# Optimization experiments

Hardware: AMD Instinct MI355X
Metric: run time of the kernel (lower is better)

The kernel has to match this reference:

```python
import jax, jax.numpy as jnp
import numpy as np

K_NEIGHBORS = 32
BN_EPS = 1e-5


def setup_inputs() -> dict:
    key = jax.random.key(0)
    ks = jax.random.split(key, 5)
    B, N, C, OUT = 16, 2048, 3, 32
    x = jax.random.normal(ks[0], (B, N, C), dtype=jnp.float32)
    W1 = jax.random.normal(ks[1], (2 * C, 2 * C), dtype=jnp.float32) * 0.3
    b1 = jax.random.normal(ks[2], (2 * C,), dtype=jnp.float32) * 0.05
    W2 = jax.random.normal(ks[3], (2 * C, OUT), dtype=jnp.float32) * 0.3
    b2 = jax.random.normal(ks[4], (OUT,), dtype=jnp.float32) * 0.05
    return {
        "x": x,
        "W1": W1, "b1": b1,
        "gamma1": jnp.ones((2 * C,), jnp.float32), "beta1": jnp.zeros((2 * C,), jnp.float32),
        "W2": W2, "b2": b2,
        "gamma2": jnp.ones((OUT,), jnp.float32), "beta2": jnp.zeros((OUT,), jnp.float32),
    }


def _batchnorm_train(h, gamma, beta):
    # normalize over all axes except the last (channel) axis, biased variance
    axes = tuple(range(h.ndim - 1))
    mean = jnp.mean(h, axis=axes)
    var = jnp.var(h, axis=axes)
    return gamma * (h - mean) * jax.lax.rsqrt(var + BN_EPS) + beta


def reference(x, W1, b1, gamma1, beta1, W2, b2, gamma2, beta2):
    B, N, C = x.shape
    K = min(K_NEIGHBORS, N)
    # brute-force KNN: squared euclidean distances [B,N,N]
    sq = jnp.sum(x * x, axis=-1)
    d = sq[:, :, None] + sq[:, None, :] - 2.0 * jnp.einsum('bnc,bmc->bnm', x, x)
    _, idx = jax.lax.top_k(-d, K)  # [B,N,K] nearest (self first)
    # gather neighbor points: [B,N,K,C]
    knn = jax.vmap(lambda pts, i: pts[i])(x, idx)
    diffs = x[:, :, None, :] - knn
    h = jnp.concatenate([jnp.broadcast_to(x[:, :, None, :], (B, N, K, C)), diffs], axis=-1)  # [B,N,K,2C]
    h = jax.nn.elu(_batchnorm_train(h @ W1 + b1, gamma1, beta1))
    h = jnp.max(h, axis=2)  # max-pool over K neighbors -> [B,N,2C]
    y = jax.nn.elu(_batchnorm_train(h @ W2 + b2, gamma2, beta2))
    return y
```

## Files before the change

### kernel.cpp

```cpp
#include <hip/hip_runtime.h>
#include <math.h>

namespace {
constexpr int NB = 16, NP = 2048, KNN = 32, CH1 = 6, CH2 = 32;
constexpr int QPB = 8;
constexpr int NBLK = NB * NP / QPB;
constexpr float BN_EPS = 1e-5f;

constexpr size_t OFF_S1REP  = 0;
constexpr size_t OFF_STATS2 = 768;
constexpr size_t OFF_SC1    = 1280;
constexpr size_t OFF_P      = 2048;
constexpr size_t OFF_MINQ   = OFF_P + sizeof(float)*NB*NP*CH1;
}

typedef __attribute__((ext_vector_type(2))) float f32x2;

__device__ __forceinline__ f32x2 pk_mul(f32x2 a, f32x2 b) {
  f32x2 d; asm("v_pk_mul_f32 %0, %1, %2" : "=v"(d) : "v"(a), "v"(b)); return d;
}
__device__ __forceinline__ f32x2 pk_add(f32x2 a, f32x2 b) {
  f32x2 d; asm("v_pk_add_f32 %0, %1, %2" : "=v"(d) : "v"(a), "v"(b)); return d;
}

template <int C> __device__ __forceinline__ int dpp0i(int x) {
  return __builtin_amdgcn_update_dpp(0, x, C, 0xf, 0xf, true);
}
template <int C> __device__ __forceinline__ float dpp0f(float x) {
  return __uint_as_float((unsigned)__builtin_amdgcn_update_dpp(
      0, (int)__float_as_uint(x), C, 0xf, 0xf, true));
}
template <int C> __device__ __forceinline__ float dppInff(float x) {
  return __uint_as_float((unsigned)__builtin_amdgcn_update_dpp(
      0x7F800000, (int)__float_as_uint(x), C, 0xf, 0xf, false));
}
__device__ __forceinline__ int wave_isum_bcast(int x) {
  x += dpp0i<0x111>(x); x += dpp0i<0x112>(x); x += dpp0i<0x114>(x);
  x += dpp0i<0x118>(x); x += dpp0i<0x142>(x); x += dpp0i<0x143>(x);
  return __builtin_amdgcn_readlane(x, 63);
}
__device__ __forceinline__ float wave_fsum63(float x) {
  x += dpp0f<0x111>(x); x += dpp0f<0x112>(x); x += dpp0f<0x114>(x);
  x += dpp0f<0x118>(x); x += dpp0f<0x142>(x); x += dpp0f<0x143>(x);
  return x;
}
__device__ __forceinline__ float wave_fmin63(float x) {
  x = fminf(x, dppInff<0x111>(x)); x = fminf(x, dppInff<0x112>(x));
  x = fminf(x, dppInff<0x114>(x)); x = fminf(x, dppInff<0x118>(x));
  x = fminf(x, dppInff<0x142>(x)); x = fminf(x, dppInff<0x143>(x));
  return x;
}

#define BSEL(m, x, y) ((((x)) & (m)) | (((y)) & ~(m)))

__global__ __launch_bounds__(512, 6) void knn_kernel(const float* __restrict__ x,
                                                     const float* __restrict__ W1,
                                                     const float* __restrict__ b1,
                                                     float* __restrict__ pout,
                                                     float* __restrict__ minq,
                                                     double* __restrict__ s1rep) {
  __shared__ f32x2 ptsX[NP/2], ptsY[NP/2], ptsZ[NP/2], ptsW[NP/2];
  __shared__ float red[12][QPB];
  const int lane = threadIdx.x & 63;
  const int w    = threadIdx.x >> 6;
  const int qi   = blockIdx.x * QPB + w;
  const int b    = qi >> 11;
  const int n    = qi & (NP - 1);

  const float* xb = x + (size_t)b * NP * 3;
  for (int k = threadIdx.x; k < NP/2; k += 512) {
    const float* p0 = xb + k*3;
    const float* p1 = xb + (k + NP/2)*3;
    float a0=p0[0], a1=p0[1], a2=p0[2];
    float c0=p1[0], c1=p1[1], c2=p1[2];
    float sa = __fadd_rn(__fadd_rn(__fmul_rn(a0,a0), __fmul_rn(a1,a1)), __fmul_rn(a2,a2));
    float sc = __fadd_rn(__fadd_rn(__fmul_rn(c0,c0), __fmul_rn(c1,c1)), __fmul_rn(c2,c2));
    ptsX[k] = (f32x2){a0, c0};
    ptsY[k] = (f32x2){a1, c1};
    ptsZ[k] = (f32x2){a2, c2};
    ptsW[k] = (f32x2){sa, sc};
  }
  __syncthreads();

  const int kq = n & (NP/2 - 1), hf = n >> 10;
  f32x2 tx = ptsX[kq], ty = ptsY[kq], tz = ptsZ[kq], tw = ptsW[kq];
  const float qx = hf ? tx.y : tx.x;
  const float qy = hf ? ty.y : ty.x;
  const float qz = hf ? tz.y : tz.x;
  const float qw = hf ? tw.y : tw.x;
  const f32x2 qx2 = {qx,qx}, qy2 = {qy,qy}, qz2 = {qz,qz}, qw2 = {qw,qw};

  unsigned d[32];
#pragma unroll
  for (int s = 0; s < 16; ++s) {
    int k = s*64 + lane;
    f32x2 X = ptsX[k], Y = ptsY[k], Z = ptsZ[k], W = ptsW[k];
    f32x2 dot = pk_add(pk_add(pk_mul(qx2, X), pk_mul(qy2, Y)), pk_mul(qz2, Z));
    f32x2 ss  = pk_add(qw2, W);
    f32x2 dt2 = pk_add(dot, dot);
    d[31 - s]  = __float_as_uint(__fsub_rn(ss.x, dt2.x));
    d[15 - s]  = __float_as_uint(__fsub_rn(ss.y, dt2.y));
  }

#pragma unroll
  for (int g = 0; g < 16; ++g) {
    unsigned hi = d[g], lo = d[g+16];
    d[g]    = __builtin_amdgcn_perm(hi, lo, 0x07060302u);
    d[g+16] = __builtin_amdgcn_perm(hi, lo, 0x05040100u);
  }
#pragma unroll
  for (int g = 0; g < 16; ++g) {
    int k = (g >> 3)*16 + (g & 7);
    unsigned hi = d[k], lo = d[k+8];
    d[k]   = __builtin_amdgcn_perm(hi, lo, 0x07030501u);
    d[k+8] = __builtin_amdgcn_perm(hi, lo, 0x06020400u);
  }
#pragma unroll
  for (int g = 0; g < 16; ++g) {
    int k = (g >> 2)*8 + (g & 3);
    unsigned A = d[k], B = d[k+4];
    d[k]   = BSEL(0x0F0F0F0Fu, B >> 4, A);
    d[k+4] = BSEL(0xF0F0F0F0u, A << 4, B);
  }
#pragma unroll
  for (int g = 0; g < 16; ++g) {
    int k = (g >> 1)*4 + (g & 1);
    unsigned A = d[k], B = d[k+2];
    d[k]   = BSEL(0x33333333u, B >> 2, A);
    d[k+2] = BSEL(0xCCCCCCCCu, A << 2, B);
  }
#pragma unroll
  for (int g = 0; g < 16; ++g) {
    int k = g*2;
    unsigned A = d[k], B = d[k+1];
    d[k]   = BSEL(0x55555555u, B >> 1, A);
    d[k+1] = BSEL(0xAAAAAAAAu, A << 1, B);
  }

  unsigned alive = 0xFFFFFFFFu, below = 0u;
  int rem = KNN, ca = 2048;
#pragma unroll
  for (int i = 1; i <= 15; ++i) {
    if (ca != rem) {
      unsigned zeros = alive & ~d[i];
      int c0 = wave_isum_bcast(__popc(zeros));
      if (c0 >= rem) { alive = zeros; ca = c0; }
      else { rem -= c0; below |= zeros; alive &= d[i]; ca -= c0; }
    }
  }
#pragma unroll
  for (int i = 16; i < 32; ++i) {
    if (ca != rem) {
      unsigned zeros = alive & ~d[i];
      int c0 = wave_isum_bcast(__popc(zeros));
      if (c0 >= rem) { alive = zeros; ca = c0; }
      else { rem -= c0; below |= zeros; alive &= d[i]; ca -= c0; }
    }
  }
  unsigned sel = below;
  if (ca == rem) {
    sel |= alive;
  } else {
    for (int v = 0; v < 32; ++v) {
      if (rem <= 0) break;
      bool mine = (alive >> v) & 1;
      unsigned long long mb = __ballot(mine);
      int c = __popcll(mb);
      if (c <= rem) { if (mine) sel |= 1u << v; rem -= c; }
      else {
        if (mine && (int)__popcll(mb & ((1ull << lane) - 1)) < rem) sel |= 1u << v;
        rem = 0;
      }
    }
  }

  float w3[CH1], w4[CH1], w5[CH1];
#pragma unroll
  for (int c = 0; c < CH1; ++c) { w3[c]=W1[3*CH1+c]; w4[c]=W1[4*CH1+c]; w5[c]=W1[5*CH1+c]; }
  float sq_[CH1], sqq[CH1], mn[CH1];
#pragma unroll
  for (int c = 0; c < CH1; ++c) { sq_[c] = 0.f; sqq[c] = 0.f; mn[c] = INFINITY; }
  unsigned m = sel;
  while (m) {
    int v = __builtin_ctz(m); m &= m - 1;
    int j = (v << 6) | lane;
    int kk = j & (NP/2 - 1);
    bool hi = v >= 16;
    f32x2 gx = ptsX[kk], gy = ptsY[kk], gz = ptsZ[kk];
    float px_ = hi ? gx.y : gx.x;
    float py_ = hi ? gy.y : gy.x;
    float pz_ = hi ? gz.y : gz.x;
#pragma unroll
    for (int c = 0; c < CH1; ++c) {
      float qv = px_*w3[c] + py_*w4[c] + pz_*w5[c];
      sq_[c] += qv; sqq[c] += qv*qv; mn[c] = fminf(mn[c], qv);
    }
  }

  float pv[CH1];
#pragma unroll
  for (int c = 0; c < CH1; ++c) {
    float qv = qx*w3[c] + qy*w4[c] + qz*w5[c];
    pv[c] = b1[c] + qx*W1[c] + qy*W1[CH1+c] + qz*W1[2*CH1+c] + qv;
  }

#pragma unroll
  for (int c = 0; c < CH1; ++c) {
    float s  = wave_fsum63(sq_[c]);
    float s2 = wave_fsum63(sqq[c]);
    float mm = wave_fmin63(mn[c]);
    if (lane == 63) {
      minq[qi*CH1 + c] = mm;
      red[c][w]       = fmaf(32.f, pv[c], -s);
      red[CH1 + c][w] = fmaf(32.f, pv[c]*pv[c], fmaf(-2.f*pv[c], s, s2));
    }
  }
  if (lane == 0) {
#pragma unroll
    for (int c = 0; c < CH1; ++c) pout[qi*CH1 + c] = pv[c];
  }
  __syncthreads();
  if (threadIdx.x < 12) {
    float s = 0.f;
#pragma unroll
    for (int ww = 0; ww < QPB; ++ww) s += red[threadIdx.x][ww];
    atomicAdd(s1rep + (blockIdx.x & 7) * 12 + threadIdx.x, (double)s);
  }
}

__global__ __launch_bounds__(128) void stage2_kernel(const float* __restrict__ p,
                                                     const float* __restrict__ minq,
                                                     const double* __restrict__ s1rep,
                                                     const float* __restrict__ gamma1,
                                                     const float* __restrict__ beta1,
                                                     const float* __restrict__ W2,
                                                     const float* __restrict__ b2,
                                                     float* __restrict__ sc1g,
                                                     double* __restrict__ stats2) {
  __shared__ double tot1[12];
  __shared__ float sc1s[12];
  __shared__ float rs[2][CH2], rq[2][CH2];
  const int t = threadIdx.x;
  if (t < 12) {
    double s = 0.0;
#pragma unroll
    for (int r = 0; r < 8; ++r) s += s1rep[r*12 + t];
    tot1[t] = s;
  }
  __syncthreads();
  if (t < CH1) {
    double cnt  = (double)NB * NP * KNN;
    double mean = tot1[t] / cnt;
    double var  = tot1[CH1 + t] / cnt - mean * mean;
    float scale = gamma1[t] / sqrtf((float)var + BN_EPS);
    sc1s[t] = scale; sc1s[CH1 + t] = beta1[t] - (float)mean * scale;
  }
  __syncthreads();
  if (blockIdx.x == 0 && t < 12) sc1g[t] = sc1s[t];

  const int qi = blockIdx.x * 128 + t;
  const int w = t >> 6, lane = t & 63;
  float me[CH1];
#pragma unroll
  for (int c = 0; c < CH1; ++c) {
    float v = fmaf(sc1s[c], p[qi*CH1 + c] - minq[qi*CH1 + c], sc1s[CH1 + c]);
    me[c] = v > 0.f ? v : expm1f(v);
  }
#pragma unroll
  for (int o = 0; o < CH2; ++o) {
    float y = b2[o];
#pragma unroll
    for (int c = 0; c < CH1; ++c) y = fmaf(me[c], W2[c*CH2 + o], y);
    float s  = wave_fsum63(y);
    float s2 = wave_fsum63(y * y);
    if (lane == 63) { rs[w][o] = s; rq[w][o] = s2; }
  }
  __syncthreads();
  if (t < CH2) atomicAdd(stats2 + t, (double)(rs[0][t] + rs[1][t]));
  else if (t < 2*CH2) atomicAdd(stats2 + t, (double)(rq[0][t-CH2] + rq[1][t-CH2]));
}

__global__ __launch_bounds__(256) void out_kernel(const float* __restrict__ p,
                                                  const float* __restrict__ minq,
                                                  const float* __restrict__ sc1,
                                                  const float* __restrict__ W2,
                                                  const float* __restrict__ b2,
                                                  const double* __restrict__ stats2,
                                                  const float* __restrict__ gamma2,
                                                  const float* __restrict__ beta2,
                                                  float* __restrict__ out) {
  __shared__ float me_lds[8][CH1];
  __shared__ float s2s[CH2], s2h[CH2];
  const int t = threadIdx.x;
  if (t < CH2) {
    double cnt  = (double)NB * NP;
    double mean = stats2[t] / cnt;
    double var  = stats2[CH2 + t] / cnt - mean * mean;
    float scale = gamma2[t] / sqrtf((float)var + BN_EPS);
    s2s[t] = scale; s2h[t] = beta2[t] - (float)mean * scale;
  }
  const int qbase = blockIdx.x * 8;
  if (t < 48) {
    int qs = t / 6, c = t % 6;
    int qi = qbase + qs;
    float v = fmaf(sc1[c], p[qi*CH1 + c] - minq[qi*CH1 + c], sc1[CH1 + c]);
    me_lds[qs][c] = v > 0.f ? v : expm1f(v);
  }
  __syncthreads();
  const int qs = t >> 5, o = t & 31;
  const int qi = qbase + qs;
  float y = b2[o];
#pragma unroll
  for (int c = 0; c < CH1; ++c) y = fmaf(me_lds[qs][c], W2[c*CH2 + o], y);
  float r = fmaf(s2s[o], y, s2h[o]);
  out[(size_t)qi*CH2 + o] = r > 0.f ? r : expm1f(r);
}

extern "C" void kernel_launch(void* const* d_in, const int* in_sizes, int n_in,
                              void* d_out, int out_size, void* d_ws, size_t ws_size,
                              hipStream_t stream) {
  const float* x      = (const float*)d_in[0];
  const float* W1     = (const float*)d_in[1];
  const float* b1     = (const float*)d_in[2];
  const float* gamma1 = (const float*)d_in[3];
  const float* beta1  = (const float*)d_in[4];
  const float* W2     = (const float*)d_in[5];
  const float* b2     = (const float*)d_in[6];
  const float* gamma2 = (const float*)d_in[7];
  const float* beta2  = (const float*)d_in[8];
  float* out = (float*)d_out;
  char* ws = (char*)d_ws;

  double* s1rep  = (double*)(ws + OFF_S1REP);
  double* stats2 = (double*)(ws + OFF_STATS2);
  float* sc1  = (float*)(ws + OFF_SC1);
  float* p    = (float*)(ws + OFF_P);
  float* minq = (float*)(ws + OFF_MINQ);

  hipMemsetAsync(ws, 0, 1280, stream);

  knn_kernel   <<<dim3(NBLK),       dim3(512), 0, stream>>>(x, W1, b1, p, minq, s1rep);
  stage2_kernel<<<dim3(NB*NP/128),  dim3(128), 0, stream>>>(p, minq, s1rep, gamma1, beta1,
                                                            W2, b2, sc1, stats2);
  out_kernel   <<<dim3(NB*NP/8),    dim3(256), 0, stream>>>(p, minq, sc1, W2, b2,
                                                            stats2, gamma2, beta2, out);
}
```

Baseline: 81.95 us.

## Use swizzled float4 shared layout, vectorized loads, and scan-based tie selection

Point data now goes through one coalesced float4 global load per thread into a swizzled float4 SoA shared-memory layout, so each lane owns 32 contiguous points and reads them with 128-bit LDS accesses. Lane-to-point ownership changes to match. The radix-select loop drops the early-exit check for its first six bits. The serial ballot-based tie-break is replaced by a wave prefix scan plus lowest-bit picks. The aim is fewer LDS instructions, fewer bank conflicts and a shorter tie-handling path, but it changes which tied candidates are chosen.

```diff
diff --git a/kernel.cpp b/kernel.cpp
--- a/kernel.cpp
+++ b/kernel.cpp
@@ -39,6 +39,11 @@
   x += dpp0i<0x118>(x); x += dpp0i<0x142>(x); x += dpp0i<0x143>(x);
   return __builtin_amdgcn_readlane(x, 63);
 }
+__device__ __forceinline__ int wave_iscan_incl(int x) {
+  x += dpp0i<0x111>(x); x += dpp0i<0x112>(x); x += dpp0i<0x114>(x);
+  x += dpp0i<0x118>(x); x += dpp0i<0x142>(x); x += dpp0i<0x143>(x);
+  return x;
+}
 __device__ __forceinline__ float wave_fsum63(float x) {
   x += dpp0f<0x111>(x); x += dpp0f<0x112>(x); x += dpp0f<0x114>(x);
   x += dpp0f<0x118>(x); x += dpp0f<0x142>(x); x += dpp0f<0x143>(x);
@@ -52,6 +57,8 @@
 }
 
 #define BSEL(m, x, y) ((((x)) & (m)) | (((y)) & ~(m)))
+
+__device__ __forceinline__ int swz(int m) { return (m & ~7) | ((m ^ (m >> 3)) & 7); }
 
 __global__ __launch_bounds__(512, 6) void knn_kernel(const float* __restrict__ x,
                                                      const float* __restrict__ W1,
@@ -59,47 +66,53 @@
                                                      float* __restrict__ pout,
                                                      float* __restrict__ minq,
                                                      double* __restrict__ s1rep) {
-  __shared__ f32x2 ptsX[NP/2], ptsY[NP/2], ptsZ[NP/2], ptsW[NP/2];
+  __shared__ float4 pts4[4 * 512];
   __shared__ float red[12][QPB];
   const int lane = threadIdx.x & 63;
   const int w    = threadIdx.x >> 6;
   const int qi   = blockIdx.x * QPB + w;
   const int b    = qi >> 11;
   const int n    = qi & (NP - 1);
+  const int s7   = lane & 7;
 
   const float* xb = x + (size_t)b * NP * 3;
-  for (int k = threadIdx.x; k < NP/2; k += 512) {
-    const float* p0 = xb + k*3;
-    const float* p1 = xb + (k + NP/2)*3;
-    float a0=p0[0], a1=p0[1], a2=p0[2];
-    float c0=p1[0], c1=p1[1], c2=p1[2];
-    float sa = __fadd_rn(__fadd_rn(__fmul_rn(a0,a0), __fmul_rn(a1,a1)), __fmul_rn(a2,a2));
-    float sc = __fadd_rn(__fadd_rn(__fmul_rn(c0,c0), __fmul_rn(c1,c1)), __fmul_rn(c2,c2));
-    ptsX[k] = (f32x2){a0, c0};
-    ptsY[k] = (f32x2){a1, c1};
-    ptsZ[k] = (f32x2){a2, c2};
-    ptsW[k] = (f32x2){sa, sc};
-  }
-  __syncthreads();
-
-  const int kq = n & (NP/2 - 1), hf = n >> 10;
-  f32x2 tx = ptsX[kq], ty = ptsY[kq], tz = ptsZ[kq], tw = ptsW[kq];
-  const float qx = hf ? tx.y : tx.x;
-  const float qy = hf ? ty.y : ty.x;
-  const float qz = hf ? tz.y : tz.x;
-  const float qw = hf ? tw.y : tw.x;
+  {
+    const int t = threadIdx.x;
+    const float4* g4 = (const float4*)xb;
+    float4 f0 = g4[t*3], f1 = g4[t*3+1], f2 = g4[t*3+2];
+    float4 X = {f0.x, f0.w, f1.z, f2.y};
+    float4 Y = {f0.y, f1.x, f1.w, f2.z};
+    float4 Z = {f0.z, f1.y, f2.x, f2.w};
+    float4 Wv;
+    Wv.x = __fadd_rn(__fadd_rn(__fmul_rn(X.x,X.x), __fmul_rn(Y.x,Y.x)), __fmul_rn(Z.x,Z.x));
+    Wv.y = __fadd_rn(__fadd_rn(__fmul_rn(X.y,X.y), __fmul_rn(Y.y,Y.y)), __fmul_rn(Z.y,Z.y));
+    Wv.z = __fadd_rn(__fadd_rn(__fmul_rn(X.z,X.z), __fmul_rn(Y.z,Y.z)), __fmul_rn(Z.z,Z.z));
+    Wv.w = __fadd_rn(__fadd_rn(__fmul_rn(X.w,X.w), __fmul_rn(Y.w,Y.w)), __fmul_rn(Z.w,Z.w));
+    const int ph = swz(t);
+    pts4[ph] = X; pts4[512+ph] = Y; pts4[1024+ph] = Z; pts4[1536+ph] = Wv;
+  }
+  __syncthreads();
+
+  const float* ps = (const float*)pts4;
+  const int fq = swz(n >> 2) * 4 + (n & 3);
+  const float qx = ps[fq], qy = ps[2048+fq], qz = ps[4096+fq], qw = ps[6144+fq];
   const f32x2 qx2 = {qx,qx}, qy2 = {qy,qy}, qz2 = {qz,qz}, qw2 = {qw,qw};
 
   unsigned d[32];
 #pragma unroll
-  for (int s = 0; s < 16; ++s) {
-    int k = s*64 + lane;
-    f32x2 X = ptsX[k], Y = ptsY[k], Z = ptsZ[k], W = ptsW[k];
-    f32x2 dot = pk_add(pk_add(pk_mul(qx2, X), pk_mul(qy2, Y)), pk_mul(qz2, Z));
-    f32x2 ss  = pk_add(qw2, W);
-    f32x2 dt2 = pk_add(dot, dot);
-    d[31 - s]  = __float_as_uint(__fsub_rn(ss.x, dt2.x));
-    d[15 - s]  = __float_as_uint(__fsub_rn(ss.y, dt2.y));
+  for (int g = 0; g < 8; ++g) {
+    const int ph = lane*8 + (g ^ s7);
+    float4 X = pts4[ph], Y = pts4[512+ph], Z = pts4[1024+ph], Wv = pts4[1536+ph];
+    f32x2 x01 = {X.x,X.y}, y01 = {Y.x,Y.y}, z01 = {Z.x,Z.y}, w01 = {Wv.x,Wv.y};
+    f32x2 x23 = {X.z,X.w}, y23 = {Y.z,Y.w}, z23 = {Z.z,Z.w}, w23 = {Wv.z,Wv.w};
+    f32x2 dotA = pk_add(pk_add(pk_mul(qx2,x01), pk_mul(qy2,y01)), pk_mul(qz2,z01));
+    f32x2 dotB = pk_add(pk_add(pk_mul(qx2,x23), pk_mul(qy2,y23)), pk_mul(qz2,z23));
+    f32x2 ssA = pk_add(qw2, w01), ssB = pk_add(qw2, w23);
+    f32x2 dA = pk_add(dotA, dotA), dB = pk_add(dotB, dotB);
+    d[31-(4*g+0)] = __float_as_uint(__fsub_rn(ssA.x, dA.x));
+    d[31-(4*g+1)] = __float_as_uint(__fsub_rn(ssA.y, dA.y));
+    d[31-(4*g+2)] = __float_as_uint(__fsub_rn(ssB.x, dB.x));
+    d[31-(4*g+3)] = __float_as_uint(__fsub_rn(ssB.y, dB.y));
   }
 
 #pragma unroll
@@ -140,37 +153,32 @@
   unsigned alive = 0xFFFFFFFFu, below = 0u;
   int rem = KNN, ca = 2048;
 #pragma unroll
-  for (int i = 1; i <= 15; ++i) {
+  for (int i = 1; i <= 6; ++i) {
+    unsigned zeros = BSEL(d[i], 0u, alive);
+    int c0 = wave_isum_bcast(__popc(zeros));
+    if (c0 >= rem) { alive = zeros; ca = c0; }
+    else { rem -= c0; below |= zeros; alive &= d[i]; ca -= c0; }
+  }
+#pragma unroll
+  for (int i = 7; i < 32; ++i) {
     if (ca != rem) {
-      unsigned zeros = alive & ~d[i];
+      unsigned zeros = BSEL(d[i], 0u, alive);
       int c0 = wave_isum_bcast(__popc(zeros));
       if (c0 >= rem) { alive = zeros; ca = c0; }
       else { rem -= c0; below |= zeros; alive &= d[i]; ca -= c0; }
     }
   }
-#pragma unroll
-  for (int i = 16; i < 32; ++i) {
-    if (ca != rem) {
-      unsigned zeros = alive & ~d[i];
-      int c0 = wave_isum_bcast(__popc(zeros));
-      if (c0 >= rem) { alive = zeros; ca = c0; }
-      else { rem -= c0; below |= zeros; alive &= d[i]; ca -= c0; }
-    }
-  }
   unsigned sel = below;
   if (ca == rem) {
     sel |= alive;
   } else {
-    for (int v = 0; v < 32; ++v) {
-      if (rem <= 0) break;
-      bool mine = (alive >> v) & 1;
-      unsigned long long mb = __ballot(mine);
-      int c = __popcll(mb);
-      if (c <= rem) { if (mine) sel |= 1u << v; rem -= c; }
-      else {
-        if (mine && (int)__popcll(mb & ((1ull << lane) - 1)) < rem) sel |= 1u << v;
-        rem = 0;
-      }
+    int cnt  = __popc(alive);
+    int excl = wave_iscan_incl(cnt) - cnt;
+    int k = rem - excl;
+    k = k < 0 ? 0 : (k > cnt ? cnt : k);
+    while (k > 0) {
+      unsigned bb = alive & (unsigned)(-(int)alive);
+      sel |= bb; alive ^= bb; --k;
     }
   }
 
@@ -183,13 +191,8 @@
   unsigned m = sel;
   while (m) {
     int v = __builtin_ctz(m); m &= m - 1;
-    int j = (v << 6) | lane;
-    int kk = j & (NP/2 - 1);
-    bool hi = v >= 16;
-    f32x2 gx = ptsX[kk], gy = ptsY[kk], gz = ptsZ[kk];
-    float px_ = hi ? gx.y : gx.x;
-    float py_ = hi ? gy.y : gy.x;
-    float pz_ = hi ? gz.y : gz.x;
+    int fi = (lane*8 + ((v >> 2) ^ s7)) * 4 + (v & 3);
+    float px_ = ps[fi], py_ = ps[2048+fi], pz_ = ps[4096+fi];
 #pragma unroll
     for (int c = 0; c < CH1; ++c) {
       float qv = px_*w3[c] + py_*w4[c] + pz_*w5[c];
```

New measurement: 81.88 us. No clear change (-0.1%).
